# Kernel tuning notes

Measured on AMD Instinct MI355X. Metric: run time of the kernel, lower is better.

The kernel has to match this reference:

```python
import jax, jax.numpy as jnp
import numpy as np

N_NODES = 100000


def _sage_conv(x, src, dst, Wl, Wr, b):
    # PyG SAGEConv (aggr='mean'): out = lin_l(mean_j x_j) + lin_r(x_i)
    deg = jax.ops.segment_sum(jnp.ones_like(src, dtype=x.dtype), dst, num_segments=N_NODES)
    agg = jax.ops.segment_sum(x[src], dst, num_segments=N_NODES)
    agg = agg / jnp.clip(deg, 1.0)[:, None]
    return agg @ Wl.T + x @ Wr.T + b


def setup_inputs() -> dict:
    key = jax.random.key(0)
    ks = jax.random.split(key, 16)
    N, E, ES = N_NODES, 1600000, 100000
    IN, H, D = 64, 128, 64

    def lin(k, out_c, in_c):
        s = 1.0 / np.sqrt(in_c)
        return jax.random.uniform(k, (out_c, in_c), jnp.float32, -s, s)

    inp = {
        "x": jax.random.normal(ks[0], (N, IN), jnp.float32),
        "edge_index": jax.random.randint(ks[1], (2, E), 0, N, jnp.int64),
        "edge_sample": jax.random.randint(ks[2], (2, ES), 0, N, jnp.int64),
        # SAGEConv 0: 64 -> 128
        "Wl0": lin(ks[3], H, IN), "Wr0": lin(ks[4], H, IN), "b0": jnp.zeros((H,), jnp.float32),
        # SAGEConv 1: 128 -> 128
        "Wl1": lin(ks[5], H, H), "Wr1": lin(ks[6], H, H), "b1": jnp.zeros((H,), jnp.float32),
        # SAGEConv 2: 128 -> 64
        "Wl2": lin(ks[7], D, H), "Wr2": lin(ks[8], D, H), "b2": jnp.zeros((D,), jnp.float32),
        # feature decoder MLP: 64 -> 128 -> 64
        "Wd1": lin(ks[9], H, D), "bd1": jnp.zeros((H,), jnp.float32),
        "Wd2": lin(ks[10], IN, H), "bd2": jnp.zeros((IN,), jnp.float32),
    }
    return inp


def reference(x, edge_index, edge_sample, Wl0, Wr0, b0, Wl1, Wr1, b1, Wl2, Wr2, b2, Wd1, bd1, Wd2, bd2):
    src, dst = edge_index[0], edge_index[1]
    # encoder (dropout = identity at inference)
    h = jax.nn.relu(_sage_conv(x, src, dst, Wl0, Wr0, b0))
    h = jax.nn.relu(_sage_conv(h, src, dst, Wl1, Wr1, b1))
    emb = _sage_conv(h, src, dst, Wl2, Wr2, b2)
    # feature decoder
    rec = jax.nn.relu(emb @ Wd1.T + bd1) @ Wd2.T + bd2
    # edge decoder: dot product
    edge_scores = jnp.sum(emb[edge_sample[0]] * emb[edge_sample[1]], axis=1)
    return emb, rec, edge_scores
```

## Files before the change

kernel.cpp:

```cpp
#include <hip/hip_runtime.h>

#define NN 100000
#define NBK 98
#define CHUNK 8192
typedef unsigned int uint;
typedef unsigned short ushort;

using f32x4 = __attribute__((ext_vector_type(4))) float;
using s16x8 = __attribute__((ext_vector_type(8))) short;

__device__ inline ushort f32_to_bf16(float f) {
  uint u = __float_as_uint(f);
  uint r = (u + 0x7FFFu + ((u >> 16) & 1u)) >> 16;
  return (ushort)r;
}
__device__ inline float bf16_to_f32(ushort h) {
  return __uint_as_float(((uint)h) << 16);
}

typedef __attribute__((address_space(1))) const unsigned int gas_u32;
typedef __attribute__((address_space(3))) unsigned int las_u32;
__device__ __forceinline__ void gld_lds16(const void* gp, void* lp) {
  __builtin_amdgcn_global_load_lds((gas_u32*)gp, (las_u32*)lp, 16, 0, 0);
}

struct P8 { const float* p[8]; };

__global__ void k_prep(const int* __restrict__ dst, uint* __restrict__ bcnt,
                       uint* __restrict__ chunkCnt, int E, int NCB,
                       const float* __restrict__ x, ushort* __restrict__ xb, int n4, int NC,
                       P8 w, ushort* __restrict__ whi, int wtotal) {
  int b = blockIdx.x;
  int tid = threadIdx.x;
  if (b < NCB) {
    __shared__ uint hist[NBK];
    for (int i = tid; i < NBK; i += 256) hist[i] = 0;
    __syncthreads();
    int base = b * CHUNK;
    int lim = min(base + CHUNK, E);
    for (int e = base + tid; e < lim; e += 256) atomicAdd(&hist[(uint)dst[e] >> 10], 1u);
    __syncthreads();
    for (int i = tid; i < NBK; i += 256) {
      uint h = hist[i];
      chunkCnt[(i << 8) + b] = h;
      if (h) atomicAdd(&bcnt[i], h);
    }
  } else if (b < NCB + NC) {
    int i = (b - NCB) * 256 + tid;
    if (i < n4) {
      float4 v = ((const float4*)x)[i];
      uint2 o;
      o.x = (uint)f32_to_bf16(v.x) | ((uint)f32_to_bf16(v.y) << 16);
      o.y = (uint)f32_to_bf16(v.z) | ((uint)f32_to_bf16(v.w) << 16);
      ((uint2*)xb)[i] = o;
    }
  } else {
    int g = (b - NCB - NC) * 256 + tid;
    if (g < wtotal) {
      const int offs[8] = {0, 8192, 16384, 32768, 49152, 57344, 65536, 73728};
      int s = 0;
#pragma unroll
      for (int i = 1; i < 8; ++i) s += (g >= offs[i]);
      whi[g] = f32_to_bf16(w.p[s][g - offs[s]]);
    }
  }
}

__global__ void k_bscan(const uint* __restrict__ bcnt, uint* __restrict__ bbase,
                        int* __restrict__ rp, const uint* __restrict__ chunkCnt,
                        uint* __restrict__ chunkBase, int NCB) {
  int bk = blockIdx.x;
  int l = threadIdx.x;
  uint p = 0, tot = 0;
  for (int i = l; i < NBK; i += 64) {
    uint v = bcnt[i];
    tot += v;
    if (i < bk) p += v;
  }
#pragma unroll
  for (int off = 1; off < 64; off <<= 1) {
    p += __shfl_xor(p, off, 64);
    tot += __shfl_xor(tot, off, 64);
  }
  if (l == 0) {
    bbase[bk] = p;
    if (bk == 0) { bbase[NBK] = tot; rp[NN] = (int)tot; }
  }
  uint carry = p;
#pragma unroll
  for (int seg = 0; seg < 4; ++seg) {
    int c = seg * 64 + l;
    uint v = (c < NCB) ? chunkCnt[(bk << 8) + c] : 0u;
    uint incl = v;
#pragma unroll
    for (int off = 1; off < 64; off <<= 1) {
      uint t = __shfl_up(incl, off, 64);
      if (l >= off) incl += t;
    }
    if (c < NCB) chunkBase[(bk << 8) + c] = carry + incl - v;
    carry += __shfl(incl, 63, 64);
  }
}

__global__ void k_bscatter(const int* __restrict__ src, const int* __restrict__ dst,
                           const uint* __restrict__ chunkBase, uint* __restrict__ packed, int E) {
  __shared__ uint cur[NBK];
  int tid = threadIdx.x;
  int b = blockIdx.x;
  for (int i = tid; i < NBK; i += 256) cur[i] = chunkBase[(i << 8) + b];
  __syncthreads();
  int base = b * CHUNK;
  int lim = min(base + CHUNK, E);
  for (int e = base + tid; e < lim; e += 256) {
    uint d = (uint)dst[e];
    uint s = (uint)src[e];
    uint bk = d >> 10;
    uint p = atomicAdd(&cur[bk], 1u);
    packed[p] = ((d & 1023u) << 20) | s;
  }
}

__global__ void k_build(const uint* __restrict__ bbase, const uint* __restrict__ packed,
                        int* __restrict__ rp, int* __restrict__ col) {
  __shared__ uint hist[1024];
  __shared__ uint ws[256];
  int b = blockIdx.x;
  int tid = threadIdx.x;
  uint lo = bbase[b], hi = bbase[b + 1];
#pragma unroll
  for (int i = 0; i < 4; ++i) hist[tid + i * 256] = 0;
  __syncthreads();
  for (uint e = lo + tid; e < hi; e += 256) atomicAdd(&hist[packed[e] >> 20], 1u);
  __syncthreads();
  uint v0 = hist[tid * 4], v1 = hist[tid * 4 + 1], v2 = hist[tid * 4 + 2], v3 = hist[tid * 4 + 3];
  ws[tid] = v0 + v1 + v2 + v3;
  __syncthreads();
  for (int off = 1; off < 256; off <<= 1) {
    uint add = (tid >= off) ? ws[tid - off] : 0u;
    __syncthreads();
    ws[tid] += add;
    __syncthreads();
  }
  uint ex = (tid > 0) ? ws[tid - 1] : 0u;
  hist[tid * 4] = ex;
  hist[tid * 4 + 1] = ex + v0;
  hist[tid * 4 + 2] = ex + v0 + v1;
  hist[tid * 4 + 3] = ex + v0 + v1 + v2;
  int nodeBase = b << 10;
#pragma unroll
  for (int i = 0; i < 4; ++i) {
    int node = nodeBase + tid * 4 + i;
    if (node < NN) rp[node] = (int)(lo + hist[tid * 4 + i]);
  }
  __syncthreads();
  for (uint e = lo + tid; e < hi; e += 256) {
    uint pk = packed[e];
    uint p = atomicAdd(&hist[pk >> 20], 1u);
    col[lo + p] = (int)(pk & 0xFFFFFu);
  }
}

#define ACC1(vv) { alo += __uint_as_float((vv) << 16); ahi += __uint_as_float((vv) & 0xffff0000u); }

template <int F, int MODE>
__global__ void k_agg(const ushort* __restrict__ x, const int* __restrict__ rp,
                      const int* __restrict__ col, const float* __restrict__ u,
                      float* __restrict__ of, ushort* __restrict__ ob, int n) {
  constexpr int RS = F / 2;
  int wave = (blockIdx.x * blockDim.x + threadIdx.x) >> 6;
  int lane = threadIdx.x & 63;
  int node, l;
  if (F == 128) { node = wave; l = lane; }
  else { node = wave * 2 + (lane >> 5); l = lane & 31; }
  if (node >= n) return;
  int beg = rp[node], end = rp[node + 1];
  int deg = end - beg;
  const uint* __restrict__ xu = (const uint*)x;
  float alo = 0.f, ahi = 0.f;
  int j = beg;
  for (; j + 8 <= end; j += 8) {
    int c0 = col[j], c1 = col[j + 1], c2 = col[j + 2], c3 = col[j + 3];
    int c4 = col[j + 4], c5 = col[j + 5], c6 = col[j + 6], c7 = col[j + 7];
    uint v0 = xu[(size_t)c0 * RS + l];
    uint v1 = xu[(size_t)c1 * RS + l];
    uint v2 = xu[(size_t)c2 * RS + l];
    uint v3 = xu[(size_t)c3 * RS + l];
    uint v4 = xu[(size_t)c4 * RS + l];
    uint v5 = xu[(size_t)c5 * RS + l];
    uint v6 = xu[(size_t)c6 * RS + l];
    uint v7 = xu[(size_t)c7 * RS + l];
    ACC1(v0) ACC1(v1) ACC1(v2) ACC1(v3) ACC1(v4) ACC1(v5) ACC1(v6) ACC1(v7)
  }
  if (j + 4 <= end) {
    int c0 = col[j], c1 = col[j + 1], c2 = col[j + 2], c3 = col[j + 3];
    uint v0 = xu[(size_t)c0 * RS + l];
    uint v1 = xu[(size_t)c1 * RS + l];
    uint v2 = xu[(size_t)c2 * RS + l];
    uint v3 = xu[(size_t)c3 * RS + l];
    ACC1(v0) ACC1(v1) ACC1(v2) ACC1(v3)
    j += 4;
  }
  for (; j < end; ++j) {
    uint v0 = xu[(size_t)col[j] * RS + l];
    ACC1(v0)
  }
  float inv = 1.0f / (float)(deg > 0 ? deg : 1);
  alo *= inv;
  ahi *= inv;
  if (MODE == 0) {
    ((uint*)ob)[(size_t)node * RS + l] = (uint)f32_to_bf16(alo) | ((uint)f32_to_bf16(ahi) << 16);
  } else {
    float2 uv = ((const float2*)u)[(size_t)node * RS + l];
    float e0 = alo + uv.x, e1 = ahi + uv.y;
    ((float2*)of)[(size_t)node * RS + l] = make_float2(e0, e1);
    ((uint*)ob)[(size_t)node * RS + l] = (uint)f32_to_bf16(e0) | ((uint)f32_to_bf16(e1) << 16);
  }
}

template <int K, bool RELU, bool DUAL, int OUTM>
__global__ __launch_bounds__(256) void k_gemm(
    const ushort* __restrict__ A, const ushort* __restrict__ Wa,
    const ushort* __restrict__ B, const ushort* __restrict__ Wb,
    const float* __restrict__ bias,
    float* __restrict__ outf, ushort* __restrict__ outb, int n) {
  constexpr int KT = 32;
  constexpr int TPP = K / KT;
  constexpr int T = (DUAL ? 2 : 1) * TPP;
  __shared__ ushort As[2][128 * KT];
  __shared__ ushort Ws[2][128 * KT];

  const int tid = threadIdx.x;
  const int lane = tid & 63;
  const int wid = tid >> 6;
  const int fr = lane & 15;
  const int fq = lane >> 4;
  const int blockRow = blockIdx.x * 128;
  const int rowBase = (wid >> 1) * 64;
  const int colBase = (wid & 1) * 64;
  const int srow = lane >> 2;
  const int sksrc = (lane & 3) ^ ((lane >> 3) & 3);
  const bool fullTile = (blockRow + 128 <= n);

  f32x4 acc[4][4];
#pragma unroll
  for (int mi = 0; mi < 4; ++mi)
#pragma unroll
    for (int ni = 0; ni < 4; ++ni) acc[mi][ni] = (f32x4){0.f, 0.f, 0.f, 0.f};

  auto stage = [&](int buf, int t) {
    const ushort* __restrict__ Ap = (DUAL && t >= TPP) ? B : A;
    const ushort* __restrict__ Wp = (DUAL && t >= TPP) ? Wb : Wa;
    const int ktb = (t % TPP) * KT;
#pragma unroll
    for (int i = 0; i < 2; ++i) {
      int r0 = (wid + i * 4) * 16;
      gld_lds16(Ap + (size_t)(blockRow + r0 + srow) * K + ktb + sksrc * 8,
                (char*)As[buf] + r0 * 64);
      gld_lds16(Wp + (size_t)(r0 + srow) * K + ktb + sksrc * 8,
                (char*)Ws[buf] + r0 * 64);
    }
  };
  auto compute = [&](int buf) {
    s16x8 af[4], wf[4];
#pragma unroll
    for (int mi = 0; mi < 4; ++mi) {
      int r = rowBase + mi * 16 + fr;
      af[mi] = *(const s16x8*)((const char*)As[buf] + r * 64 + ((fq ^ ((r >> 1) & 3)) << 4));
    }
#pragma unroll
    for (int ni = 0; ni < 4; ++ni) {
      int r = colBase + ni * 16 + fr;
      wf[ni] = *(const s16x8*)((const char*)Ws[buf] + r * 64 + ((fq ^ ((r >> 1) & 3)) << 4));
    }
#pragma unroll
    for (int mi = 0; mi < 4; ++mi)
#pragma unroll
      for (int ni = 0; ni < 4; ++ni)
        acc[mi][ni] = __builtin_amdgcn_mfma_f32_16x16x32_bf16(af[mi], wf[ni], acc[mi][ni], 0, 0, 0);
  };

  if (fullTile) {
    stage(0, 0);
#pragma unroll
    for (int t = 0; t < T; ++t) {
      if (t + 1 < T) {
        stage((t + 1) & 1, t + 1);
        asm volatile("s_waitcnt vmcnt(4)" ::: "memory");
      } else {
        asm volatile("s_waitcnt vmcnt(0)" ::: "memory");
      }
      __builtin_amdgcn_sched_barrier(0);
      __builtin_amdgcn_s_barrier();
      compute(t & 1);
      if (t + 1 < T) __builtin_amdgcn_s_barrier();
    }
  } else {
#pragma unroll
    for (int t = 0; t < T; ++t) {
      const ushort* __restrict__ Ap = (DUAL && t >= TPP) ? B : A;
      const ushort* __restrict__ Wp = (DUAL && t >= TPP) ? Wb : Wa;
      const int ktb = (t % TPP) * KT;
      __syncthreads();
      for (int c = tid; c < 128 * 4; c += 256) {
        int r = c >> 2, s = c & 3;
        int row = blockRow + r;
        int ds = s ^ ((r >> 1) & 3);
        uint4 v = make_uint4(0u, 0u, 0u, 0u);
        if (row < n) v = *(const uint4*)(Ap + (size_t)row * K + ktb + s * 8);
        *(uint4*)((char*)As[0] + r * 64 + (ds << 4)) = v;
        *(uint4*)((char*)Ws[0] + r * 64 + (ds << 4)) =
            *(const uint4*)(Wp + (size_t)r * K + ktb + s * 8);
      }
      __syncthreads();
      compute(0);
    }
  }

#pragma unroll
  for (int mi = 0; mi < 4; ++mi) {
#pragma unroll
    for (int ni = 0; ni < 4; ++ni) {
#pragma unroll
      for (int r = 0; r < 4; ++r) {
        int row = blockRow + rowBase + mi * 16 + fq * 4 + r;
        int colI = colBase + ni * 16 + fr;
        if (row < n) {
          float v = acc[mi][ni][r];
          if (OUTM == 3) {
            if (colI < 64)
              outb[(size_t)row * 64 + colI] = f32_to_bf16(v);
            else
              outf[(size_t)row * 64 + (colI - 64)] = v + bias[colI - 64];
          } else {
            if (bias) v += bias[colI];
            if (RELU) v = fmaxf(v, 0.f);
            outb[(size_t)row * 128 + colI] = f32_to_bf16(v);
          }
        }
      }
    }
  }
}

__global__ __launch_bounds__(256) void k_dec(
    const ushort* __restrict__ emb, const ushort* __restrict__ Wd1,
    const float* __restrict__ bd1, const ushort* __restrict__ Wd2,
    const float* __restrict__ bd2, float* __restrict__ rec, int n) {
  __shared__ ushort smem[24 * 1024];
  ushort* As = smem;
  ushort* W1 = smem + 8192;
  ushort* W2 = smem + 16384;
  ushort* Hs = smem;

  const int tid = threadIdx.x;
  const int lane = tid & 63;
  const int wid = tid >> 6;
  const int fr = lane & 15;
  const int fq = lane >> 4;
  const int blockRow = blockIdx.x * 128;
  const int rowBase1 = (wid >> 1) * 64;
  const int colBase1 = (wid & 1) * 64;
  const int srow8 = lane >> 3, sl8 = lane & 7;
  const int srow4 = lane >> 4, sl16 = lane & 15;
  const bool fullTile = (blockRow + 128 <= n);

  if (fullTile) {
#pragma unroll
    for (int i = 0; i < 4; ++i) {
      int r0 = (wid + i * 4) * 8;
      gld_lds16(emb + (size_t)(blockRow + r0 + srow8) * 64 + (sl8 ^ srow8) * 8,
                (char*)As + r0 * 128);
    }
#pragma unroll
    for (int i = 0; i < 4; ++i) {
      int r0 = (wid + i * 4) * 8;
      gld_lds16(Wd1 + (size_t)(r0 + srow8) * 64 + (sl8 ^ srow8) * 8, (char*)W1 + r0 * 128);
    }
#pragma unroll
    for (int i = 0; i < 4; ++i) {
      int r0 = (wid + i * 4) * 4;
      int grow = r0 + srow4;
      gld_lds16(Wd2 + (size_t)grow * 128 + (sl16 ^ (grow & 7)) * 8, (char*)W2 + r0 * 256);
    }
  } else {
    for (int c = tid; c < 128 * 8; c += 256) {
      int r = c >> 3, s = c & 7;
      int row = blockRow + r;
      uint4 v = make_uint4(0u, 0u, 0u, 0u);
      if (row < n) v = *(const uint4*)(emb + (size_t)row * 64 + s * 8);
      *(uint4*)((char*)As + r * 128 + ((s ^ (r & 7)) << 4)) = v;
    }
    for (int c = tid; c < 128 * 8; c += 256) {
      int r = c >> 3, s = c & 7;
      *(uint4*)((char*)W1 + r * 128 + ((s ^ (r & 7)) << 4)) =
          *(const uint4*)(Wd1 + (size_t)r * 64 + s * 8);
    }
    for (int c = tid; c < 64 * 16; c += 256) {
      int r = c >> 4, s = c & 15;
      *(uint4*)((char*)W2 + r * 256 + ((s ^ (r & 7)) << 4)) =
          *(const uint4*)(Wd2 + (size_t)r * 128 + s * 8);
    }
  }
  __syncthreads();

  f32x4 a1[4][4];
#pragma unroll
  for (int mi = 0; mi < 4; ++mi)
#pragma unroll
    for (int ni = 0; ni < 4; ++ni) a1[mi][ni] = (f32x4){0.f, 0.f, 0.f, 0.f};
#pragma unroll
  for (int ks = 0; ks < 2; ++ks) {
    s16x8 af[4], wf[4];
#pragma unroll
    for (int mi = 0; mi < 4; ++mi) {
      int r = rowBase1 + mi * 16 + fr;
      af[mi] = *(const s16x8*)((const char*)As + r * 128 + (((ks * 4 + fq) ^ (r & 7)) << 4));
    }
#pragma unroll
    for (int ni = 0; ni < 4; ++ni) {
      int r = colBase1 + ni * 16 + fr;
      wf[ni] = *(const s16x8*)((const char*)W1 + r * 128 + (((ks * 4 + fq) ^ (r & 7)) << 4));
    }
#pragma unroll
    for (int mi = 0; mi < 4; ++mi)
#pragma unroll
      for (int ni = 0; ni < 4; ++ni)
        a1[mi][ni] = __builtin_amdgcn_mfma_f32_16x16x32_bf16(af[mi], wf[ni], a1[mi][ni], 0, 0, 0);
  }
  __syncthreads();
#pragma unroll
  for (int mi = 0; mi < 4; ++mi) {
#pragma unroll
    for (int ni = 0; ni < 4; ++ni) {
#pragma unroll
      for (int r = 0; r < 4; ++r) {
        int rowl = rowBase1 + mi * 16 + fq * 4 + r;
        int colI = colBase1 + ni * 16 + fr;
        float v = fmaxf(a1[mi][ni][r] + bd1[colI], 0.f);
        int byte = rowl * 256 + ((((colI >> 3) ^ (rowl & 7))) << 4) + (colI & 7) * 2;
        *(ushort*)((char*)Hs + byte) = f32_to_bf16(v);
      }
    }
  }
  __syncthreads();

  f32x4 a2[2][4];
#pragma unroll
  for (int mi = 0; mi < 2; ++mi)
#pragma unroll
    for (int ni = 0; ni < 4; ++ni) a2[mi][ni] = (f32x4){0.f, 0.f, 0.f, 0.f};
#pragma unroll
  for (int kk = 0; kk < 4; ++kk) {
    s16x8 af[2], wf[4];
#pragma unroll
    for (int mi = 0; mi < 2; ++mi) {
      int r = wid * 32 + mi * 16 + fr;
      af[mi] = *(const s16x8*)((const char*)Hs + r * 256 + (((kk * 4 + fq) ^ (r & 7)) << 4));
    }
#pragma unroll
    for (int ni = 0; ni < 4; ++ni) {
      int r = ni * 16 + fr;
      wf[ni] = *(const s16x8*)((const char*)W2 + r * 256 + (((kk * 4 + fq) ^ (r & 7)) << 4));
    }
#pragma unroll
    for (int mi = 0; mi < 2; ++mi)
#pragma unroll
      for (int ni = 0; ni < 4; ++ni)
        a2[mi][ni] = __builtin_amdgcn_mfma_f32_16x16x32_bf16(af[mi], wf[ni], a2[mi][ni], 0, 0, 0);
  }
#pragma unroll
  for (int mi = 0; mi < 2; ++mi) {
#pragma unroll
    for (int ni = 0; ni < 4; ++ni) {
#pragma unroll
      for (int r = 0; r < 4; ++r) {
        int row = blockRow + wid * 32 + mi * 16 + fq * 4 + r;
        int colI = ni * 16 + fr;
        if (row < n) rec[(size_t)row * 64 + colI] = a2[mi][ni][r] + bd2[colI];
      }
    }
  }
}

__global__ void k_dot(const float* __restrict__ emb, const int* __restrict__ ea,
                      const int* __restrict__ eb, float* __restrict__ out, int ne) {
  int hw = (blockIdx.x * blockDim.x + threadIdx.x) >> 5;
  int l = threadIdx.x & 31;
  if (hw >= ne) return;
  float2 a = ((const float2*)(emb + (size_t)ea[hw] * 64))[l];
  float2 b = ((const float2*)(emb + (size_t)eb[hw] * 64))[l];
  float v = a.x * b.x + a.y * b.y;
#pragma unroll
  for (int off = 16; off; off >>= 1) v += __shfl_xor(v, off, 64);
  if (l == 0) out[hw] = v;
}

extern "C" void kernel_launch(void* const* d_in, const int* in_sizes, int n_in,
                              void* d_out, int out_size, void* d_ws, size_t ws_size,
                              hipStream_t stream) {
  const float* x = (const float*)d_in[0];
  const int* ei = (const int*)d_in[1];
  const int* es = (const int*)d_in[2];
  const float* b0 = (const float*)d_in[5];
  const float* b1 = (const float*)d_in[8];
  const float* b2 = (const float*)d_in[11];
  const float* bd1 = (const float*)d_in[13];
  const float* bd2 = (const float*)d_in[15];

  const int E = in_sizes[1] / 2;
  const int ES = in_sizes[2] / 2;
  const int* srcv = ei;
  const int* dstv = ei + E;
  const int* ea = es;
  const int* eb = es + ES;

  char* wp = (char*)d_ws;
  auto alloc = [&](size_t bytes) {
    char* p = wp;
    wp += (bytes + 511) & ~(size_t)511;
    return p;
  };
  int* row_ptr = (int*)alloc((NN + 1) * sizeof(int));
  uint* bcnt = (uint*)alloc(NBK * sizeof(uint));
  uint* bbase = (uint*)alloc((NBK + 1) * sizeof(uint));
  uint* chunkCnt = (uint*)alloc((size_t)NBK * 256 * sizeof(uint));
  uint* chunkBase = (uint*)alloc((size_t)NBK * 256 * sizeof(uint));
  uint* packed = (uint*)alloc((size_t)E * sizeof(uint));
  int* colv = (int*)alloc((size_t)E * sizeof(int));
  ushort* xb = (ushort*)alloc((size_t)NN * 64 * 2);
  ushort* aggb = (ushort*)alloc((size_t)NN * 128 * 2);
  ushort* h1b = (ushort*)alloc((size_t)NN * 128 * 2);
  ushort* h2b = (ushort*)alloc((size_t)NN * 128 * 2);
  float* uf = (float*)alloc((size_t)NN * 64 * 4);
  ushort* embb = (ushort*)alloc((size_t)NN * 64 * 2);
  ushort* Whb = (ushort*)alloc(81920 * 2);

  const int WO0 = 0, WO1 = 8192, WO2 = 16384, WO3 = 32768, WO4 = 49152,
            WO6 = 65536, WO7 = 73728;

  float* out_emb = (float*)d_out;
  float* out_rec = out_emb + (size_t)NN * 64;
  float* out_sc = out_rec + (size_t)NN * 64;

  hipMemsetAsync(bcnt, 0, NBK * sizeof(uint), stream);

  P8 wptrs;
  wptrs.p[0] = (const float*)d_in[3];  wptrs.p[1] = (const float*)d_in[4];
  wptrs.p[2] = (const float*)d_in[6];  wptrs.p[3] = (const float*)d_in[7];
  wptrs.p[4] = (const float*)d_in[9];  wptrs.p[5] = (const float*)d_in[10];
  wptrs.p[6] = (const float*)d_in[12]; wptrs.p[7] = (const float*)d_in[14];

  const int NCB = (E + CHUNK - 1) / CHUNK;
  const int n4 = NN * 64 / 4;
  const int NC = (n4 + 255) / 256;
  const int NS = (81920 + 255) / 256;
  k_prep<<<NCB + NC + NS, 256, 0, stream>>>(dstv, bcnt, chunkCnt, E, NCB, x, xb, n4, NC,
                                            wptrs, Whb, 81920);
  k_bscan<<<NBK, 64, 0, stream>>>(bcnt, bbase, row_ptr, chunkCnt, chunkBase, NCB);
  k_bscatter<<<NCB, 256, 0, stream>>>(srcv, dstv, chunkBase, packed, E);
  k_build<<<NBK, 256, 0, stream>>>(bbase, packed, row_ptr, colv);

  const int g64 = (NN + 7) / 8;
  const int g128a = (NN + 3) / 4;
  dim3 gg((NN + 127) / 128);

  k_agg<64, 0><<<g64, 256, 0, stream>>>(xb, row_ptr, colv, nullptr, nullptr, aggb, NN);
  k_gemm<64, true, true, 0><<<gg, 256, 0, stream>>>(
      aggb, Whb + WO0, xb, Whb + WO1, b0, nullptr, h1b, NN);
  k_agg<128, 0><<<g128a, 256, 0, stream>>>(h1b, row_ptr, colv, nullptr, nullptr, aggb, NN);
  k_gemm<128, true, true, 0><<<gg, 256, 0, stream>>>(
      aggb, Whb + WO2, h1b, Whb + WO3, b1, nullptr, h2b, NN);
  k_gemm<128, false, false, 3><<<gg, 256, 0, stream>>>(
      h2b, Whb + WO4, nullptr, nullptr, b2, uf, aggb, NN);
  k_agg<64, 2><<<g64, 256, 0, stream>>>(aggb, row_ptr, colv, uf, out_emb, embb, NN);
  k_dec<<<gg, 256, 0, stream>>>(embb, Whb + WO6, bd1, Whb + WO7, bd2, out_rec, NN);
  k_dot<<<(ES + 7) / 8, 256, 0, stream>>>(out_emb, ea, eb, out_sc, ES);
}
```

Measured before the change: 340.3 us.

## Halve GEMM row tile, double CSR buckets, store root term in bf16

Three unrelated changes. The GEMM row tile drops from 128 to 64 rows, doubling block count and halving accumulator registers to help occupancy on the 100k-row problem. The CSR build splits destinations into 196 buckets of 512 nodes instead of 98 of 1024, giving more blocks and a smaller LDS histogram. The layer-2 root term is now stored as bf16 instead of fp32, halving that intermediate's write and read traffic at some precision cost.

```diff
diff --git a/kernel.cpp b/kernel.cpp
--- a/kernel.cpp
+++ b/kernel.cpp
@@ -1,7 +1,7 @@
 #include <hip/hip_runtime.h>
 
 #define NN 100000
-#define NBK 98
+#define NBK 196
 #define CHUNK 8192
 typedef unsigned int uint;
 typedef unsigned short ushort;
@@ -38,7 +38,7 @@
     __syncthreads();
     int base = b * CHUNK;
     int lim = min(base + CHUNK, E);
-    for (int e = base + tid; e < lim; e += 256) atomicAdd(&hist[(uint)dst[e] >> 10], 1u);
+    for (int e = base + tid; e < lim; e += 256) atomicAdd(&hist[(uint)dst[e] >> 9], 1u);
     __syncthreads();
     for (int i = tid; i < NBK; i += 256) {
       uint h = hist[i];
@@ -114,26 +114,26 @@
   for (int e = base + tid; e < lim; e += 256) {
     uint d = (uint)dst[e];
     uint s = (uint)src[e];
-    uint bk = d >> 10;
+    uint bk = d >> 9;
     uint p = atomicAdd(&cur[bk], 1u);
-    packed[p] = ((d & 1023u) << 20) | s;
+    packed[p] = ((d & 511u) << 20) | s;
   }
 }
 
 __global__ void k_build(const uint* __restrict__ bbase, const uint* __restrict__ packed,
                         int* __restrict__ rp, int* __restrict__ col) {
-  __shared__ uint hist[1024];
+  __shared__ uint hist[512];
   __shared__ uint ws[256];
   int b = blockIdx.x;
   int tid = threadIdx.x;
   uint lo = bbase[b], hi = bbase[b + 1];
-#pragma unroll
-  for (int i = 0; i < 4; ++i) hist[tid + i * 256] = 0;
+  hist[tid] = 0;
+  hist[tid + 256] = 0;
   __syncthreads();
   for (uint e = lo + tid; e < hi; e += 256) atomicAdd(&hist[packed[e] >> 20], 1u);
   __syncthreads();
-  uint v0 = hist[tid * 4], v1 = hist[tid * 4 + 1], v2 = hist[tid * 4 + 2], v3 = hist[tid * 4 + 3];
-  ws[tid] = v0 + v1 + v2 + v3;
+  uint v0 = hist[tid * 2], v1 = hist[tid * 2 + 1];
+  ws[tid] = v0 + v1;
   __syncthreads();
   for (int off = 1; off < 256; off <<= 1) {
     uint add = (tid >= off) ? ws[tid - off] : 0u;
@@ -142,15 +142,13 @@
     __syncthreads();
   }
   uint ex = (tid > 0) ? ws[tid - 1] : 0u;
-  hist[tid * 4] = ex;
-  hist[tid * 4 + 1] = ex + v0;
-  hist[tid * 4 + 2] = ex + v0 + v1;
-  hist[tid * 4 + 3] = ex + v0 + v1 + v2;
-  int nodeBase = b << 10;
-#pragma unroll
-  for (int i = 0; i < 4; ++i) {
-    int node = nodeBase + tid * 4 + i;
-    if (node < NN) rp[node] = (int)(lo + hist[tid * 4 + i]);
+  hist[tid * 2] = ex;
+  hist[tid * 2 + 1] = ex + v0;
+  int nodeBase = b << 9;
+#pragma unroll
+  for (int i = 0; i < 2; ++i) {
+    int node = nodeBase + tid * 2 + i;
+    if (node < NN) rp[node] = (int)(lo + hist[tid * 2 + i]);
   }
   __syncthreads();
   for (uint e = lo + tid; e < hi; e += 256) {
@@ -164,7 +162,7 @@
 
 template <int F, int MODE>
 __global__ void k_agg(const ushort* __restrict__ x, const int* __restrict__ rp,
-                      const int* __restrict__ col, const float* __restrict__ u,
+                      const int* __restrict__ col, const ushort* __restrict__ u,
                       float* __restrict__ of, ushort* __restrict__ ob, int n) {
   constexpr int RS = F / 2;
   int wave = (blockIdx.x * blockDim.x + threadIdx.x) >> 6;
@@ -210,8 +208,9 @@
   if (MODE == 0) {
     ((uint*)ob)[(size_t)node * RS + l] = (uint)f32_to_bf16(alo) | ((uint)f32_to_bf16(ahi) << 16);
   } else {
-    float2 uv = ((const float2*)u)[(size_t)node * RS + l];
-    float e0 = alo + uv.x, e1 = ahi + uv.y;
+    uint uv = ((const uint*)u)[(size_t)node * RS + l];
+    float e0 = alo + __uint_as_float(uv << 16);
+    float e1 = ahi + __uint_as_float(uv & 0xffff0000u);
     ((float2*)of)[(size_t)node * RS + l] = make_float2(e0, e1);
     ((uint*)ob)[(size_t)node * RS + l] = (uint)f32_to_bf16(e0) | ((uint)f32_to_bf16(e1) << 16);
   }
@@ -222,11 +221,12 @@
     const ushort* __restrict__ A, const ushort* __restrict__ Wa,
     const ushort* __restrict__ B, const ushort* __restrict__ Wb,
     const float* __restrict__ bias,
-    float* __restrict__ outf, ushort* __restrict__ outb, int n) {
+    ushort* __restrict__ outu, ushort* __restrict__ outb, int n) {
+  constexpr int BM = 64;
   constexpr int KT = 32;
   constexpr int TPP = K / KT;
   constexpr int T = (DUAL ? 2 : 1) * TPP;
-  __shared__ ushort As[2][128 * KT];
+  __shared__ ushort As[2][BM * KT];
   __shared__ ushort Ws[2][128 * KT];
 
   const int tid = threadIdx.x;
@@ -234,16 +234,16 @@
   const int wid = tid >> 6;
   const int fr = lane & 15;
   const int fq = lane >> 4;
-  const int blockRow = blockIdx.x * 128;
-  const int rowBase = (wid >> 1) * 64;
+  const int blockRow = blockIdx.x * BM;
+  const int rowBase = (wid >> 1) * 32;
   const int colBase = (wid & 1) * 64;
   const int srow = lane >> 2;
   const int sksrc = (lane & 3) ^ ((lane >> 3) & 3);
-  const bool fullTile = (blockRow + 128 <= n);
-
-  f32x4 acc[4][4];
-#pragma unroll
-  for (int mi = 0; mi < 4; ++mi)
+  const bool fullTile = (blockRow + BM <= n);
+
+  f32x4 acc[2][4];
+#pragma unroll
+  for (int mi = 0; mi < 2; ++mi)
 #pragma unroll
     for (int ni = 0; ni < 4; ++ni) acc[mi][ni] = (f32x4){0.f, 0.f, 0.f, 0.f};
 
@@ -251,19 +251,22 @@
     const ushort* __restrict__ Ap = (DUAL && t >= TPP) ? B : A;
     const ushort* __restrict__ Wp = (DUAL && t >= TPP) ? Wb : Wa;
     const int ktb = (t % TPP) * KT;
+    {
+      int r0 = wid * 16;
+      gld_lds16(Ap + (size_t)(blockRow + r0 + srow) * K + ktb + sksrc * 8,
+                (char*)As[buf] + r0 * 64);
+    }
 #pragma unroll
     for (int i = 0; i < 2; ++i) {
       int r0 = (wid + i * 4) * 16;
-      gld_lds16(Ap + (size_t)(blockRow + r0 + srow) * K + ktb + sksrc * 8,
-                (char*)As[buf] + r0 * 64);
       gld_lds16(Wp + (size_t)(r0 + srow) * K + ktb + sksrc * 8,
                 (char*)Ws[buf] + r0 * 64);
     }
   };
   auto compute = [&](int buf) {
-    s16x8 af[4], wf[4];
-#pragma unroll
-    for (int mi = 0; mi < 4; ++mi) {
+    s16x8 af[2], wf[4];
+#pragma unroll
+    for (int mi = 0; mi < 2; ++mi) {
       int r = rowBase + mi * 16 + fr;
       af[mi] = *(const s16x8*)((const char*)As[buf] + r * 64 + ((fq ^ ((r >> 1) & 3)) << 4));
     }
@@ -273,7 +276,7 @@
       wf[ni] = *(const s16x8*)((const char*)Ws[buf] + r * 64 + ((fq ^ ((r >> 1) & 3)) << 4));
     }
 #pragma unroll
-    for (int mi = 0; mi < 4; ++mi)
+    for (int mi = 0; mi < 2; ++mi)
 #pragma unroll
       for (int ni = 0; ni < 4; ++ni)
         acc[mi][ni] = __builtin_amdgcn_mfma_f32_16x16x32_bf16(af[mi], wf[ni], acc[mi][ni], 0, 0, 0);
@@ -285,7 +288,7 @@
     for (int t = 0; t < T; ++t) {
       if (t + 1 < T) {
         stage((t + 1) & 1, t + 1);
-        asm volatile("s_waitcnt vmcnt(4)" ::: "memory");
+        asm volatile("s_waitcnt vmcnt(3)" ::: "memory");
       } else {
         asm volatile("s_waitcnt vmcnt(0)" ::: "memory");
       }
@@ -301,13 +304,18 @@
       const ushort* __restrict__ Wp = (DUAL && t >= TPP) ? Wb : Wa;
       const int ktb = (t % TPP) * KT;
       __syncthreads();
-      for (int c = tid; c < 128 * 4; c += 256) {
+      {
+        int c = tid;
         int r = c >> 2, s = c & 3;
         int row = blockRow + r;
         int ds = s ^ ((r >> 1) & 3);
         uint4 v = make_uint4(0u, 0u, 0u, 0u);
         if (row < n) v = *(const uint4*)(Ap + (size_t)row * K + ktb + s * 8);
         *(uint4*)((char*)As[0] + r * 64 + (ds << 4)) = v;
+      }
+      for (int c = tid; c < 128 * 4; c += 256) {
+        int r = c >> 2, s = c & 3;
+        int ds = s ^ ((r >> 1) & 3);
         *(uint4*)((char*)Ws[0] + r * 64 + (ds << 4)) =
             *(const uint4*)(Wp + (size_t)r * K + ktb + s * 8);
       }
@@ -317,7 +325,7 @@
   }
 
 #pragma unroll
-  for (int mi = 0; mi < 4; ++mi) {
+  for (int mi = 0; mi < 2; ++mi) {
 #pragma unroll
     for (int ni = 0; ni < 4; ++ni) {
 #pragma unroll
@@ -330,7 +338,7 @@
             if (colI < 64)
               outb[(size_t)row * 64 + colI] = f32_to_bf16(v);
             else
-              outf[(size_t)row * 64 + (colI - 64)] = v + bias[colI - 64];
+              outu[(size_t)row * 64 + (colI - 64)] = f32_to_bf16(v + bias[colI - 64]);
           } else {
             if (bias) v += bias[colI];
             if (RELU) v = fmaxf(v, 0.f);
@@ -531,7 +539,7 @@
   ushort* aggb = (ushort*)alloc((size_t)NN * 128 * 2);
   ushort* h1b = (ushort*)alloc((size_t)NN * 128 * 2);
   ushort* h2b = (ushort*)alloc((size_t)NN * 128 * 2);
-  float* uf = (float*)alloc((size_t)NN * 64 * 4);
+  ushort* ub = (ushort*)alloc((size_t)NN * 64 * 2);
   ushort* embb = (ushort*)alloc((size_t)NN * 64 * 2);
   ushort* Whb = (ushort*)alloc(81920 * 2);
 
@@ -562,7 +570,7 @@
 
   const int g64 = (NN + 7) / 8;
   const int g128a = (NN + 3) / 4;
-  dim3 gg((NN + 127) / 128);
+  dim3 gg((NN + 63) / 64);
 
   k_agg<64, 0><<<g64, 256, 0, stream>>>(xb, row_ptr, colv, nullptr, nullptr, aggb, NN);
   k_gemm<64, true, true, 0><<<gg, 256, 0, stream>>>(
@@ -571,8 +579,8 @@
   k_gemm<128, true, true, 0><<<gg, 256, 0, stream>>>(
       aggb, Whb + WO2, h1b, Whb + WO3, b1, nullptr, h2b, NN);
   k_gemm<128, false, false, 3><<<gg, 256, 0, stream>>>(
-      h2b, Whb + WO4, nullptr, nullptr, b2, uf, aggb, NN);
-  k_agg<64, 2><<<g64, 256, 0, stream>>>(aggb, row_ptr, colv, uf, out_emb, embb, NN);
-  k_dec<<<gg, 256, 0, stream>>>(embb, Whb + WO6, bd1, Whb + WO7, bd2, out_rec, NN);
+      h2b, Whb + WO4, nullptr, nullptr, b2, ub, aggb, NN);
+  k_agg<64, 2><<<g64, 256, 0, stream>>>(aggb, row_ptr, colv, ub, out_emb, embb, NN);
+  k_dec<<<(NN + 127) / 128, 256, 0, stream>>>(embb, Whb + WO6, bd1, Whb + WO7, bd2, out_rec, NN);
   k_dot<<<(ES + 7) / 8, 256, 0, stream>>>(out_emb, ea, eb, out_sc, ES);
 }
```

Result: faster. 297.6 us (median of 2 runs) (-12.6%).
